# Optimization experiments

Hardware: AMD Instinct MI355X
Metric: run time of the kernel (lower is better)

## Reference

```python
import jax, jax.numpy as jnp
import numpy as np

B, T, U = 64, 800, 80          # batch, stroke timesteps, char sequence length
IN, H, V = 3, 400, 57          # input_dim, hidden_dim, onehot_dim (vocab)
K, G = 10, 20                  # n_window, n_gaussian
D1 = H + IN + V                # input dim of recurrent layers >= 1


def setup_inputs() -> dict:
    key = jax.random.key(0)
    ks = jax.random.split(key, 12)
    std = 0.075
    nrm = lambda k, shp: (std * jax.random.normal(k, shp)).astype(jnp.float32)
    char_ids = jax.random.randint(ks[1], (B, U), 0, V)
    return {
        "x_input": jax.random.normal(ks[0], (B, T, IN), jnp.float32),
        "onehot": jax.nn.one_hot(char_ids, V, dtype=jnp.float32),
        "h0": jnp.zeros((B, H), jnp.float32),
        "h1": jnp.zeros((B, H), jnp.float32),
        "h2": jnp.zeros((B, H), jnp.float32),
        # GRU layer 0 (input: strokes only)
        "W_ih0": nrm(ks[2], (3 * H, IN)), "W_hh0": nrm(ks[3], (3 * H, H)),
        "b_ih0": jnp.zeros((3 * H,), jnp.float32), "b_hh0": jnp.zeros((3 * H,), jnp.float32),
        # GRU layer 1 (shared by all layers >= 1, faithful to the torch code which
        # always calls self.rnn_layer1 in the loop)
        "W_ih1": nrm(ks[4], (3 * H, D1)), "W_hh1": nrm(ks[5], (3 * H, H)),
        "b_ih1": jnp.zeros((3 * H,), jnp.float32), "b_hh1": jnp.zeros((3 * H,), jnp.float32),
        # attention window linear: hidden -> 3*K (alpha, beta, kappa); bias ~ N(-4, 0.1)
        "W_win": nrm(ks[6], (3 * K, H)),
        "b_win": (-4.0 + 0.1 * jax.random.normal(ks[7], (3 * K,))).astype(jnp.float32),
        # MDN head: hidden -> 1 + 6*G
        "W_mdn": nrm(ks[8], (1 + 6 * G, H)),
        "b_mdn": jnp.zeros((1 + 6 * G,), jnp.float32),
    }


def gru(x, h0, W_ih, W_hh, b_ih, b_hh):
    """PyTorch-convention GRU. x: (B,T,D), h0: (B,H) -> (out (B,T,H), hT (B,H))."""
    xg = jnp.einsum('btd,gd->btg', x, W_ih) + b_ih  # (B,T,3H), precomputed input gates

    def step(h, xg_t):
        gh = h @ W_hh.T + b_hh
        xr, xz, xn = jnp.split(xg_t, 3, axis=-1)
        hr, hz, hn = jnp.split(gh, 3, axis=-1)
        r = jax.nn.sigmoid(xr + hr)
        z = jax.nn.sigmoid(xz + hz)
        n = jnp.tanh(xn + r * hn)
        h_new = (1.0 - z) * n + z * h
        return h_new, h_new

    hT, outs = jax.lax.scan(step, h0, jnp.swapaxes(xg, 0, 1))
    return jnp.swapaxes(outs, 0, 1), hT


def reference(x_input, onehot, h0, h1, h2,
              W_ih0, W_hh0, b_ih0, b_hh0,
              W_ih1, W_hh1, b_ih1, b_hh1,
              W_win, b_win, W_mdn, b_mdn):
    out0, _ = gru(x_input, h0, W_ih0, W_hh0, b_ih0, b_hh0)  # (B,T,H)

    # Graves attention window (training=True path: running_kappa = cumsum(kappa))
    abk = jnp.exp(out0 @ W_win.T + b_win)                    # (B,T,3K)
    alpha, beta, kappa = jnp.split(abk, 3, axis=-1)          # each (B,T,K)
    running_kappa = jnp.cumsum(kappa, axis=1)                # (B,T,K)
    u = jnp.arange(onehot.shape[1], dtype=x_input.dtype)     # (U,)
    diff = running_kappa[..., None] - u                      # (B,T,K,U)
    phi = jnp.sum(alpha[..., None] * jnp.exp(-beta[..., None] * diff * diff), axis=2)  # (B,T,U)
    window = jnp.einsum('btu,buv->btv', phi, onehot)         # (B,T,V)

    # layers >= 1 all use layer-1 weights (faithful to original torch code)
    out = jnp.concatenate([out0, window, x_input], axis=-1)
    out, _ = gru(out, h1, W_ih1, W_hh1, b_ih1, b_hh1)
    out = jnp.concatenate([out, window, x_input], axis=-1)
    out, _ = gru(out, h2, W_ih1, W_hh1, b_ih1, b_hh1)

    mdn = out.reshape(-1, H) @ W_mdn.T + b_mdn               # (B*T, 1+6G)
    pi_logit = mdn[:, 0 * G:1 * G]
    mu1 = mdn[:, 1 * G:2 * G]
    mu2 = mdn[:, 2 * G:3 * G]
    log_sigma1 = mdn[:, 3 * G:4 * G]
    log_sigma2 = mdn[:, 4 * G:5 * G]
    rho = jnp.tanh(mdn[:, 5 * G:6 * G])
    e_logit = mdn[:, 6 * G:]
    return jnp.concatenate([pi_logit, mu1, mu2, log_sigma1, log_sigma2, rho, e_logit], axis=-1)
```

## Files before the change

### kernel.cpp

```cpp
#include <hip/hip_runtime.h>
#include <math.h>

#define Bx 64
#define Tx 800
#define Ux 80
#define INx 3
#define Hx 400
#define Vx 57
#define Kx 10


typedef float v2f __attribute__((ext_vector_type(2)));
typedef float v4f __attribute__((ext_vector_type(4)));

__device__ __forceinline__ float sigf(float x) { return 1.f / (1.f + expf(-x)); }

__device__ __forceinline__ void pk_lo(v2f& acc, v2f w, v2f h) {
    asm("v_pk_fma_f32 %0, %1, %2, %0 op_sel:[0,0,0] op_sel_hi:[0,1,1]"
        : "+v"(acc) : "v"(w), "v"(h));
}
__device__ __forceinline__ void pk_hi(v2f& acc, v2f w, v2f h) {
    asm("v_pk_fma_f32 %0, %1, %2, %0 op_sel:[1,0,0] op_sel_hi:[1,1,1]"
        : "+v"(acc) : "v"(w), "v"(h));
}

__global__ void k_zero(int* __restrict__ cnt) {
    int i = blockIdx.x * blockDim.x + threadIdx.x;
    if (i < 3 * 16 * 32) cnt[i] = 0;
}

__global__ void k_transpose_x(const float* __restrict__ x, float* __restrict__ xT) {
    int idx = blockIdx.x * blockDim.x + threadIdx.x;
    if (idx >= Tx * INx * Bx) return;
    int b = idx & 63;
    int d = (idx >> 6) % INx;
    int t = idx / (64 * INx);
    xT[idx] = x[((size_t)b * Tx + t) * INx + d];
}

__global__ void k_transpose_oh(const float* __restrict__ oh, float* __restrict__ ohT) {
    int idx = blockIdx.x * blockDim.x + threadIdx.x;
    if (idx >= Ux * Vx * Bx) return;
    int b = idx & 63;
    int uv = idx >> 6;
    int v = uv % Vx;
    int u = uv / Vx;
    ohT[idx] = oh[((size_t)b * Ux + u) * Vx + v];
}

__global__ void k_packW(const float* __restrict__ Whh, const float* __restrict__ Wih,
                        float* __restrict__ Wp, int NP, int xcols) {
    int idx = blockIdx.x * blockDim.x + threadIdx.x;
    int total = 16 * 3 * NP * 400;
    if (idx >= total) return;
    int q = idx % 400;
    int m = (idx / 400) % (3 * NP);
    int us = idx / (400 * 3 * NP);
    int g = m / NP, p = m % NP;
    int s = q / 25, u = q % 25;
    int row = g * 400 + us * 25 + u;
    float v0, v1;
    if (p < 13) {
        int kl0 = 2 * p, kl1 = 2 * p + 1;
        v0 = (kl0 < 25) ? Whh[(size_t)row * 400 + s * 25 + kl0] : 0.f;
        v1 = (kl1 < 25) ? Whh[(size_t)row * 400 + s * 25 + kl1] : 0.f;
    } else {
        int jx0 = 2 * (p - 13), jx1 = jx0 + 1;
        int kx0 = s * 29 + jx0, kx1 = s * 29 + jx1;
        v0 = (jx0 < 29 && kx0 < xcols) ? Wih[(size_t)row * xcols + kx0] : 0.f;
        v1 = (jx1 < 29 && kx1 < xcols) ? Wih[(size_t)row * xcols + kx1] : 0.f;
    }
    Wp[(size_t)idx * 2]     = v0;
    Wp[(size_t)idx * 2 + 1] = v1;
}

template <int XP>
__global__ __launch_bounds__(448, 1) void k_rec(
    const float* __restrict__ Wp, const float* __restrict__ prev,
    const float* __restrict__ winb, const float* __restrict__ xT,
    const float* __restrict__ hinit, const float* __restrict__ Wih_small,
    const float* __restrict__ bih, const float* __restrict__ bhh,
    float* __restrict__ outL, int* __restrict__ cnt) {
    constexpr int NP = 13 + XP;
    constexpr int XW = (XP > 0) ? 466 : 4;
    __shared__ __align__(16) float xcat_h[404 * 4];
    __shared__ __align__(16) float xcat_x[2][XW * 4];
    __shared__ __align__(16) float hprev[2][104 * 4];
    __shared__ v2f red2[8 * 400];
    __shared__ float biasLDS[150];
    __shared__ float wih0LDS[225];

    const int tid = threadIdx.x;
    const int us = blockIdx.x & 15;
    const int cg = blockIdx.x >> 4;
    const int cb = cg * 4;
    const int U0 = us * 25;
    const int q = tid;
    const int s = q / 25;
    int* cnt_cg = cnt + cg * 32;

    v2f wr[NP], wz[NP], wn[NP];
    if (q < 400) {
        const v2f* Wp2 = (const v2f*)Wp;
        const size_t base = (size_t)(us * 3 * NP) * 400 + q;
        #pragma unroll
        for (int m = 0; m < NP; ++m) {
            wr[m] = Wp2[base + (size_t)m * 400];
            wz[m] = Wp2[base + (size_t)(NP + m) * 400];
            wn[m] = Wp2[base + (size_t)(2 * NP + m) * 400];
        }
    } else {
        #pragma unroll
        for (int m = 0; m < NP; ++m) {
            wr[m] = (v2f){0.f, 0.f}; wz[m] = (v2f){0.f, 0.f}; wn[m] = (v2f){0.f, 0.f};
        }
    }
    #pragma unroll
    for (int m = 0; m < NP; ++m) {
        asm volatile("" : "+v"(wr[m]));
        asm volatile("" : "+v"(wz[m]));
        asm volatile("" : "+v"(wn[m]));
    }
    if (tid < 75)        biasLDS[tid] = bih[(tid / 25) * 400 + U0 + (tid % 25)];
    else if (tid < 150)  biasLDS[tid] = bhh[((tid - 75) / 25) * 400 + U0 + ((tid - 75) % 25)];
    if (XP == 0 && tid < 225) {
        int u = tid / 9, r9 = tid % 9, g = r9 / 3, d = r9 % 3;
        wih0LDS[tid] = Wih_small[(size_t)(g * 400 + U0 + u) * 3 + d];
    }
    for (int k = tid; k < 404; k += 448)
        *(v4f*)&xcat_h[k * 4] = (v4f){0.f, 0.f, 0.f, 0.f};
    for (int k = tid; k < 2 * XW; k += 448)
        *(v4f*)&xcat_x[0][k * 4] = (v4f){0.f, 0.f, 0.f, 0.f};

    if (XP > 0) {
        for (int kx = tid; kx < 460; kx += 448) {
            v4f xv;
            if (kx < 400)      xv = *(const v4f*)(prev + (size_t)kx * 64 + cb);
            else if (kx < 457) xv = *(const v4f*)(winb + (size_t)(kx - 400) * 64 + cb);
            else               xv = *(const v4f*)(xT + (size_t)(kx - 457) * 64 + cb);
            *(v4f*)&xcat_x[0][kx * 4] = xv;
        }
    } else {
        if (tid < 3)
            *(v4f*)&xcat_x[0][tid * 4] = *(const v4f*)(xT + (size_t)tid * 64 + cb);
    }

    for (int t = 0; t < Tx; ++t) {
        const int pl = t & 1;
        if (t > 0) {
            if (tid < 64) {
                int* fp = cnt_cg + (tid & 15);
                int fv = __hip_atomic_load(fp, __ATOMIC_RELAXED, __HIP_MEMORY_SCOPE_AGENT);
                while (!__all(fv >= t)) {
                    __builtin_amdgcn_s_sleep(1);
                    fv = __hip_atomic_load(fp, __ATOMIC_RELAXED, __HIP_MEMORY_SCOPE_AGENT);
                }
            }
            __syncthreads();
        }
        if (tid < 400) {
            v4f hv;
            if (t == 0) {
                hv.x = hinit[(size_t)(cb + 0) * 400 + tid];
                hv.y = hinit[(size_t)(cb + 1) * 400 + tid];
                hv.z = hinit[(size_t)(cb + 2) * 400 + tid];
                hv.w = hinit[(size_t)(cb + 3) * 400 + tid];
            } else {
                const float* hp0 = outL + (size_t)(t - 1) * 25600 + (size_t)tid * 64 + cb;
                asm volatile("global_load_dwordx4 %0, %1, off sc0 sc1"
                             : "=v"(hv) : "v"(hp0) : "memory");
                asm volatile("s_waitcnt vmcnt(0)" ::: "memory");
            }
            *(v4f*)&xcat_h[tid * 4] = hv;
            int d = tid - U0;
            if ((unsigned)d < 25u) *(v4f*)&hprev[t & 1][d * 4] = hv;
        }
        __syncthreads();

        if (q < 400) {
            v2f aR0 = {0, 0}, aR1 = {0, 0}, aZ0 = {0, 0}, aZ1 = {0, 0};
            v2f aHN0 = {0, 0}, aHN1 = {0, 0}, aXN0 = {0, 0}, aXN1 = {0, 0};
            const float* hb = &xcat_h[s * 100];
            #pragma unroll
            for (int p = 0; p < 13; ++p) {
                v2f a01 = *(const v2f*)(hb + 8 * p);
                v2f a23 = *(const v2f*)(hb + 8 * p + 2);
                v2f b01 = *(const v2f*)(hb + 8 * p + 4);
                v2f b23 = *(const v2f*)(hb + 8 * p + 6);
                v2f r_ = wr[p], z_ = wz[p], n_ = wn[p];
                pk_lo(aR0, r_, a01);  pk_lo(aR1, r_, a23);
                pk_hi(aR0, r_, b01);  pk_hi(aR1, r_, b23);
                pk_lo(aZ0, z_, a01);  pk_lo(aZ1, z_, a23);
                pk_hi(aZ0, z_, b01);  pk_hi(aZ1, z_, b23);
                pk_lo(aHN0, n_, a01); pk_lo(aHN1, n_, a23);
                pk_hi(aHN0, n_, b01); pk_hi(aHN1, n_, b23);
            }
            if (XP > 0) {
                const float* xb = &xcat_x[pl][s * 29 * 4];
                #pragma unroll
                for (int p = 0; p < XP; ++p) {
                    v2f a01 = *(const v2f*)(xb + 8 * p);
                    v2f a23 = *(const v2f*)(xb + 8 * p + 2);
                    v2f b01 = *(const v2f*)(xb + 8 * p + 4);
                    v2f b23 = *(const v2f*)(xb + 8 * p + 6);
                    v2f r_ = wr[13 + p], z_ = wz[13 + p], n_ = wn[13 + p];
                    pk_lo(aR0, r_, a01);  pk_lo(aR1, r_, a23);
                    pk_hi(aR0, r_, b01);  pk_hi(aR1, r_, b23);
                    pk_lo(aZ0, z_, a01);  pk_lo(aZ1, z_, a23);
                    pk_hi(aZ0, z_, b01);  pk_hi(aZ1, z_, b23);
                    pk_lo(aXN0, n_, a01); pk_lo(aXN1, n_, a23);
                    pk_hi(aXN0, n_, b01); pk_hi(aXN1, n_, b23);
                }
            }
            red2[0 * 400 + q] = aR0;  red2[1 * 400 + q] = aR1;
            red2[2 * 400 + q] = aZ0;  red2[3 * 400 + q] = aZ1;
            red2[4 * 400 + q] = aHN0; red2[5 * 400 + q] = aHN1;
            red2[6 * 400 + q] = aXN0; red2[7 * 400 + q] = aXN1;
        }
        __syncthreads();

        if (tid < 64) {
            #pragma unroll
            for (int rep = 0; rep < 2; ++rep) {
                int o = tid + rep * 64;
                if (o < 100) {
                    int u = o >> 2, c = o & 3;
                    int half = c >> 1, e = c & 1;
                    const float* redf = (const float*)red2;
                    float R = 0, Z = 0, HN = 0, XN = 0;
                    #pragma unroll 4
                    for (int s2 = 0; s2 < 16; ++s2) {
                        int idx = s2 * 25 + u;
                        R  += redf[((0 + half) * 400 + idx) * 2 + e];
                        Z  += redf[((2 + half) * 400 + idx) * 2 + e];
                        HN += redf[((4 + half) * 400 + idx) * 2 + e];
                        XN += redf[((6 + half) * 400 + idx) * 2 + e];
                    }
                    R += biasLDS[u] + biasLDS[75 + u];
                    Z += biasLDS[25 + u] + biasLDS[100 + u];
                    XN += biasLDS[50 + u];
                    HN += biasLDS[125 + u];
                    if (XP == 0) {
                        #pragma unroll
                        for (int d = 0; d < 3; ++d) {
                            float xv = xcat_x[pl][d * 4 + c];
                            R  += wih0LDS[u * 9 + 0 + d] * xv;
                            Z  += wih0LDS[u * 9 + 3 + d] * xv;
                            XN += wih0LDS[u * 9 + 6 + d] * xv;
                        }
                    }
                    float r = sigf(R);
                    float z = sigf(Z);
                    float n = tanhf(XN + r * HN);
                    float hp = hprev[t & 1][u * 4 + c];
                    float hnew = (1.f - z) * n + z * hp;
                    __hip_atomic_store(outL + (size_t)t * 25600 + (size_t)(U0 + u) * 64 + cb + c,
                                       hnew, __ATOMIC_RELAXED, __HIP_MEMORY_SCOPE_AGENT);
                }
            }
            asm volatile("s_waitcnt vmcnt(0)" ::: "memory");
            if (tid == 0)
                __hip_atomic_store(cnt_cg + us, t + 1,
                                   __ATOMIC_RELAXED, __HIP_MEMORY_SCOPE_AGENT);
        } else if (t + 1 < Tx) {
            const int p2 = (t + 1) & 1;
            if (XP > 0) {
                for (int kx = tid - 64; kx < 460; kx += 384) {
                    v4f xv;
                    if (kx < 400)      xv = *(const v4f*)(prev + (size_t)(t + 1) * 25600 + kx * 64 + cb);
                    else if (kx < 457) xv = *(const v4f*)(winb + (size_t)(t + 1) * 3648 + (kx - 400) * 64 + cb);
                    else               xv = *(const v4f*)(xT + (size_t)(t + 1) * 192 + (kx - 457) * 64 + cb);
                    *(v4f*)&xcat_x[p2][kx * 4] = xv;
                }
            } else {
                if (tid < 67) {
                    int d = tid - 64;
                    *(v4f*)&xcat_x[p2][d * 4] = *(const v4f*)(xT + (size_t)(t + 1) * 192 + d * 64 + cb);
                }
            }
        }
    }
}

__global__ __launch_bounds__(256) void k_abk(const float* __restrict__ out0,
    const float* __restrict__ Wwin, const float* __restrict__ bwin,
    float* __restrict__ abk) {
    int t = blockIdx.x;
    int b = threadIdx.x & 63;
    int js = threadIdx.x >> 6;
    int j0 = js * 8;
    int nj = min(8, 30 - j0);
    float acc[8];
    for (int i = 0; i < nj; i++) acc[i] = bwin[j0 + i];
    const float* o = out0 + (size_t)t * 25600;
    for (int k = 0; k < Hx; k++) {
        float hv = o[k * 64 + b];
        for (int i = 0; i < nj; i++) acc[i] += Wwin[(j0 + i) * Hx + k] * hv;
    }
    for (int i = 0; i < nj; i++)
        abk[(size_t)t * 1920 + (j0 + i) * 64 + b] = expf(acc[i]);
}

__global__ void k_cumsum(float* __restrict__ abk) {
    int tid = blockIdx.x * blockDim.x + threadIdx.x;
    if (tid >= Kx * Bx) return;
    int b = tid & 63;
    int k = tid >> 6;
    float run = 0.f;
    size_t base = (size_t)(20 + k) * 64 + b;
    for (int t = 0; t < Tx; t++) {
        size_t i = (size_t)t * 1920 + base;
        run += abk[i];
        abk[i] = run;
    }
}

__global__ __launch_bounds__(256) void k_window(const float* __restrict__ abk,
    const float* __restrict__ ohT, float* __restrict__ win) {
    int t = blockIdx.x;
    int b = threadIdx.x & 63;
    int sub = threadIdx.x >> 6;
    __shared__ float phi[Ux][64];

    float al[Kx], be[Kx], kc[Kx];
    const float* ab = abk + (size_t)t * 1920;
    #pragma unroll
    for (int k = 0; k < Kx; k++) {
        al[k] = ab[k * 64 + b];
        be[k] = ab[(10 + k) * 64 + b];
        kc[k] = ab[(20 + k) * 64 + b];
    }
    for (int u = sub * 20; u < sub * 20 + 20; u++) {
        float ssum = 0.f;
        float uf = (float)u;
        #pragma unroll
        for (int k = 0; k < Kx; k++) {
            float d = kc[k] - uf;
            ssum += al[k] * __expf(-be[k] * d * d);
        }
        phi[u][b] = ssum;
    }
    __syncthreads();

    int v0 = sub * 15;
    int nv = min(15, Vx - v0);
    float acc[15];
    for (int i = 0; i < nv; i++) acc[i] = 0.f;
    for (int u = 0; u < Ux; u++) {
        float pv = phi[u][b];
        const float* oh = ohT + (size_t)(u * Vx) * 64;
        for (int i = 0; i < nv; i++) acc[i] += pv * oh[(v0 + i) * 64 + b];
    }
    for (int i = 0; i < nv; i++)
        win[(size_t)t * 3648 + (v0 + i) * 64 + b] = acc[i];
}

__global__ __launch_bounds__(256) void k_mdn(const float* __restrict__ out2,
    const float* __restrict__ Wm, const float* __restrict__ bm,
    float* __restrict__ out) {
    int t = blockIdx.x;
    int b = threadIdx.x & 63;
    int js = threadIdx.x >> 6;
    int j0 = js * 31;
    int nj = min(31, 121 - j0);
    float acc[31];
    for (int i = 0; i < nj; i++) acc[i] = bm[j0 + i];
    const float* o = out2 + (size_t)t * 25600;
    for (int k = 0; k < Hx; k += 4) {
        float i0 = o[k * 64 + b];
        float i1 = o[(k + 1) * 64 + b];
        float i2 = o[(k + 2) * 64 + b];
        float i3 = o[(k + 3) * 64 + b];
        for (int i = 0; i < nj; i++) {
            const float* wp = Wm + (size_t)(j0 + i) * Hx + k;
            float4 qv = *(const float4*)wp;
            acc[i] += qv.x * i0 + qv.y * i1 + qv.z * i2 + qv.w * i3;
        }
    }
    size_t rb = ((size_t)b * Tx + t) * 121;
    for (int i = 0; i < nj; i++) {
        int j = j0 + i;
        float v = acc[i];
        if (j >= 100 && j < 120) v = tanhf(v);
        out[rb + j] = v;
    }
}

extern "C" void kernel_launch(void* const* d_in, const int* in_sizes, int n_in,
                              void* d_out, int out_size, void* d_ws, size_t ws_size,
                              hipStream_t stream) {
    const float* x    = (const float*)d_in[0];
    const float* oneh = (const float*)d_in[1];
    const float* h0i  = (const float*)d_in[2];
    const float* h1i  = (const float*)d_in[3];
    const float* h2i  = (const float*)d_in[4];
    const float* Wih0 = (const float*)d_in[5];
    const float* Whh0 = (const float*)d_in[6];
    const float* bih0 = (const float*)d_in[7];
    const float* bhh0 = (const float*)d_in[8];
    const float* Wih1 = (const float*)d_in[9];
    const float* Whh1 = (const float*)d_in[10];
    const float* bih1 = (const float*)d_in[11];
    const float* bhh1 = (const float*)d_in[12];
    const float* Wwin = (const float*)d_in[13];
    const float* bwin = (const float*)d_in[14];
    const float* Wmdn = (const float*)d_in[15];
    const float* bmdn = (const float*)d_in[16];

    float* ws    = (float*)d_ws;
    float* out0  = ws;
    float* out12 = ws + 20480000;
    float* winb  = ws + 40960000;
    float* abk   = ws + 43878400;
    float* xT    = ws + 45414400;
    float* ohT   = ws + 45568000;
    float* Wp0   = ws + 45859840;
    float* Wp12  = ws + 46359040;
    int*   cnt   = (int*)(ws + 47434240);

    hipLaunchKernelGGL(k_zero, dim3(6), dim3(256), 0, stream, cnt);
    hipLaunchKernelGGL(k_transpose_x, dim3((Tx * INx * Bx + 255) / 256), dim3(256), 0, stream, x, xT);
    hipLaunchKernelGGL(k_transpose_oh, dim3((Ux * Vx * Bx + 255) / 256), dim3(256), 0, stream, oneh, ohT);
    hipLaunchKernelGGL(k_packW, dim3((16 * 3 * 13 * 400 + 255) / 256), dim3(256), 0, stream,
                       Whh0, Wih0, Wp0, 13, 3);
    hipLaunchKernelGGL(k_packW, dim3((16 * 3 * 28 * 400 + 255) / 256), dim3(256), 0, stream,
                       Whh1, Wih1, Wp12, 28, 460);

    hipLaunchKernelGGL((k_rec<0>), dim3(256), dim3(448), 0, stream,
                       Wp0, (const float*)nullptr, (const float*)nullptr, xT,
                       h0i, Wih0, bih0, bhh0, out0, cnt + 0 * 512);

    hipLaunchKernelGGL(k_abk, dim3(Tx), dim3(256), 0, stream, out0, Wwin, bwin, abk);
    hipLaunchKernelGGL(k_cumsum, dim3(10), dim3(64), 0, stream, abk);
    hipLaunchKernelGGL(k_window, dim3(Tx), dim3(256), 0, stream, abk, ohT, winb);

    hipLaunchKernelGGL((k_rec<15>), dim3(256), dim3(448), 0, stream,
                       Wp12, out0, winb, xT, h1i, (const float*)nullptr,
                       bih1, bhh1, out12, cnt + 1 * 512);
    hipLaunchKernelGGL((k_rec<15>), dim3(256), dim3(448), 0, stream,
                       Wp12, out12, winb, xT, h2i, (const float*)nullptr,
                       bih1, bhh1, out0, cnt + 2 * 512);

    hipLaunchKernelGGL(k_mdn, dim3(Tx), dim3(256), 0, stream, out0, Wmdn, bmdn, (float*)d_out);
}
```

Before: 13.39 ms.

## Fuse GRU layers 1 and 2 into one wavefront-pipelined persistent kernel

Layers 1 and 2 of the GRU recurrence now run concurrently in a single 512-block launch. Each layer-2 block spins on layer-1 progress counters so that it stays about two timesteps behind layer 1, rather than waiting for layer 1 to finish all 800 steps. Layer-2 reads of layer-1 output use cache-bypassing loads, and the old generic k_rec path loses its XP>0 branches. This needs all 512 blocks to be co-resident to avoid deadlock, and it puts more pressure on the memory system through the cross-layer polling.

```diff
diff --git a/kernel.cpp b/kernel.cpp
--- a/kernel.cpp
+++ b/kernel.cpp
@@ -22,6 +22,23 @@
 __device__ __forceinline__ void pk_hi(v2f& acc, v2f w, v2f h) {
     asm("v_pk_fma_f32 %0, %1, %2, %0 op_sel:[1,0,0] op_sel_hi:[1,1,1]"
         : "+v"(acc) : "v"(w), "v"(h));
+}
+
+__device__ __forceinline__ v4f load1_sc(const float* p) {
+    v4f r;
+    asm volatile("global_load_dwordx4 %0, %1, off sc0 sc1\n\t"
+                 "s_waitcnt vmcnt(0)"
+                 : "=v"(r) : "v"(p) : "memory");
+    return r;
+}
+__device__ __forceinline__ void load2_sc(v4f& a, v4f& b,
+                                         const float* pa, const float* pb) {
+    asm volatile("global_load_dwordx4 %0, %2, off sc0 sc1\n\t"
+                 "global_load_dwordx4 %1, %3, off sc0 sc1\n\t"
+                 "s_waitcnt vmcnt(0)"
+                 : "=&v"(a), "=&v"(b)
+                 : "v"(pa), "v"(pb)
+                 : "memory");
 }
 
 __global__ void k_zero(int* __restrict__ cnt) {
@@ -115,12 +132,6 @@
             wr[m] = (v2f){0.f, 0.f}; wz[m] = (v2f){0.f, 0.f}; wn[m] = (v2f){0.f, 0.f};
         }
     }
-    #pragma unroll
-    for (int m = 0; m < NP; ++m) {
-        asm volatile("" : "+v"(wr[m]));
-        asm volatile("" : "+v"(wz[m]));
-        asm volatile("" : "+v"(wn[m]));
-    }
     if (tid < 75)        biasLDS[tid] = bih[(tid / 25) * 400 + U0 + (tid % 25)];
     else if (tid < 150)  biasLDS[tid] = bhh[((tid - 75) / 25) * 400 + U0 + ((tid - 75) % 25)];
     if (XP == 0 && tid < 225) {
@@ -132,15 +143,7 @@
     for (int k = tid; k < 2 * XW; k += 448)
         *(v4f*)&xcat_x[0][k * 4] = (v4f){0.f, 0.f, 0.f, 0.f};
 
-    if (XP > 0) {
-        for (int kx = tid; kx < 460; kx += 448) {
-            v4f xv;
-            if (kx < 400)      xv = *(const v4f*)(prev + (size_t)kx * 64 + cb);
-            else if (kx < 457) xv = *(const v4f*)(winb + (size_t)(kx - 400) * 64 + cb);
-            else               xv = *(const v4f*)(xT + (size_t)(kx - 457) * 64 + cb);
-            *(v4f*)&xcat_x[0][kx * 4] = xv;
-        }
-    } else {
+    if (XP == 0) {
         if (tid < 3)
             *(v4f*)&xcat_x[0][tid * 4] = *(const v4f*)(xT + (size_t)tid * 64 + cb);
     }
@@ -166,10 +169,7 @@
                 hv.z = hinit[(size_t)(cb + 2) * 400 + tid];
                 hv.w = hinit[(size_t)(cb + 3) * 400 + tid];
             } else {
-                const float* hp0 = outL + (size_t)(t - 1) * 25600 + (size_t)tid * 64 + cb;
-                asm volatile("global_load_dwordx4 %0, %1, off sc0 sc1"
-                             : "=v"(hv) : "v"(hp0) : "memory");
-                asm volatile("s_waitcnt vmcnt(0)" ::: "memory");
+                hv = load1_sc(outL + (size_t)(t - 1) * 25600 + (size_t)tid * 64 + cb);
             }
             *(v4f*)&xcat_h[tid * 4] = hv;
             int d = tid - U0;
@@ -194,23 +194,6 @@
                 pk_hi(aZ0, z_, b01);  pk_hi(aZ1, z_, b23);
                 pk_lo(aHN0, n_, a01); pk_lo(aHN1, n_, a23);
                 pk_hi(aHN0, n_, b01); pk_hi(aHN1, n_, b23);
-            }
-            if (XP > 0) {
-                const float* xb = &xcat_x[pl][s * 29 * 4];
-                #pragma unroll
-                for (int p = 0; p < XP; ++p) {
-                    v2f a01 = *(const v2f*)(xb + 8 * p);
-                    v2f a23 = *(const v2f*)(xb + 8 * p + 2);
-                    v2f b01 = *(const v2f*)(xb + 8 * p + 4);
-                    v2f b23 = *(const v2f*)(xb + 8 * p + 6);
-                    v2f r_ = wr[13 + p], z_ = wz[13 + p], n_ = wn[13 + p];
-                    pk_lo(aR0, r_, a01);  pk_lo(aR1, r_, a23);
-                    pk_hi(aR0, r_, b01);  pk_hi(aR1, r_, b23);
-                    pk_lo(aZ0, z_, a01);  pk_lo(aZ1, z_, a23);
-                    pk_hi(aZ0, z_, b01);  pk_hi(aZ1, z_, b23);
-                    pk_lo(aXN0, n_, a01); pk_lo(aXN1, n_, a23);
-                    pk_hi(aXN0, n_, b01); pk_hi(aXN1, n_, b23);
-                }
             }
             red2[0 * 400 + q] = aR0;  red2[1 * 400 + q] = aR1;
             red2[2 * 400 + q] = aZ0;  red2[3 * 400 + q] = aZ1;
@@ -263,19 +246,225 @@
                 __hip_atomic_store(cnt_cg + us, t + 1,
                                    __ATOMIC_RELAXED, __HIP_MEMORY_SCOPE_AGENT);
         } else if (t + 1 < Tx) {
-            const int p2 = (t + 1) & 1;
-            if (XP > 0) {
-                for (int kx = tid - 64; kx < 460; kx += 384) {
-                    v4f xv;
-                    if (kx < 400)      xv = *(const v4f*)(prev + (size_t)(t + 1) * 25600 + kx * 64 + cb);
-                    else if (kx < 457) xv = *(const v4f*)(winb + (size_t)(t + 1) * 3648 + (kx - 400) * 64 + cb);
-                    else               xv = *(const v4f*)(xT + (size_t)(t + 1) * 192 + (kx - 457) * 64 + cb);
-                    *(v4f*)&xcat_x[p2][kx * 4] = xv;
-                }
-            } else {
+            if (XP == 0) {
                 if (tid < 67) {
                     int d = tid - 64;
-                    *(v4f*)&xcat_x[p2][d * 4] = *(const v4f*)(xT + (size_t)(t + 1) * 192 + d * 64 + cb);
+                    *(v4f*)&xcat_x[(t + 1) & 1][d * 4] =
+                        *(const v4f*)(xT + (size_t)(t + 1) * 192 + d * 64 + cb);
+                }
+            }
+        }
+    }
+}
+
+__device__ __forceinline__ const float* xaddr(int kx, int tt, int cb,
+    const float* prev, const float* winb, const float* xT) {
+    if (kx < 400)      return prev + (size_t)tt * 25600 + (size_t)kx * 64 + cb;
+    else if (kx < 457) return winb + (size_t)tt * 3648 + (size_t)(kx - 400) * 64 + cb;
+    else               return xT   + (size_t)tt * 192  + (size_t)(kx - 457) * 64 + cb;
+}
+
+__global__ __attribute__((amdgpu_flat_work_group_size(448, 448), amdgpu_waves_per_eu(4)))
+void k_rec12(
+    const float* __restrict__ Wp, float* __restrict__ out0,
+    float* __restrict__ out12, const float* __restrict__ winb,
+    const float* __restrict__ xT, const float* __restrict__ h1i,
+    const float* __restrict__ h2i, const float* __restrict__ bih,
+    const float* __restrict__ bhh, int* __restrict__ cnt) {
+    constexpr int NP = 28;
+    constexpr int XW = 466;
+    __shared__ __align__(16) float xcat_h[404 * 4];
+    __shared__ __align__(16) float xcat_x[2][XW * 4];
+    __shared__ __align__(16) float hprev[2][104 * 4];
+    __shared__ v2f red2[8 * 400];
+    __shared__ float biasLDS[150];
+
+    const int tid = threadIdx.x;
+    const int lay = blockIdx.x >> 8;
+    const int blk = blockIdx.x & 255;
+    const int us = blk & 15;
+    const int cg = blk >> 4;
+    const int cb = cg * 4;
+    const int U0 = us * 25;
+    const int q = tid;
+    const int s = q / 25;
+
+    const float* prev  = lay ? out12 : out0;
+    float* outL        = lay ? out0  : out12;
+    const float* hinit = lay ? h2i   : h1i;
+    int* cntOwn = cnt + (lay ? 1024 : 512) + cg * 32;
+    int* cntDep = cnt + 512 + cg * 32;
+
+    v2f wr[NP], wz[NP], wn[NP];
+    if (q < 400) {
+        const v2f* Wp2 = (const v2f*)Wp;
+        const size_t base = (size_t)(us * 3 * NP) * 400 + q;
+        #pragma unroll
+        for (int m = 0; m < NP; ++m) {
+            wr[m] = Wp2[base + (size_t)m * 400];
+            wz[m] = Wp2[base + (size_t)(NP + m) * 400];
+            wn[m] = Wp2[base + (size_t)(2 * NP + m) * 400];
+        }
+    } else {
+        #pragma unroll
+        for (int m = 0; m < NP; ++m) {
+            wr[m] = (v2f){0.f, 0.f}; wz[m] = (v2f){0.f, 0.f}; wn[m] = (v2f){0.f, 0.f};
+        }
+    }
+    if (tid < 75)        biasLDS[tid] = bih[(tid / 25) * 400 + U0 + (tid % 25)];
+    else if (tid < 150)  biasLDS[tid] = bhh[((tid - 75) / 25) * 400 + U0 + ((tid - 75) % 25)];
+    for (int k = tid; k < 404; k += 448)
+        *(v4f*)&xcat_h[k * 4] = (v4f){0.f, 0.f, 0.f, 0.f};
+    for (int k = tid; k < 2 * XW; k += 448)
+        *(v4f*)&xcat_x[0][k * 4] = (v4f){0.f, 0.f, 0.f, 0.f};
+
+    for (int t = 0; t < Tx; ++t) {
+        const int pl = t & 1;
+        if (t > 0 || lay) {
+            if (tid < 64) {
+                int i16 = tid & 15;
+                const bool mine = ((tid >> 4) & 1) == 0;
+                int* fp = mine ? (cntOwn + i16) : (cntDep + i16);
+                int tdep = t + 2; if (tdep > Tx) tdep = Tx;
+                const int tgt = mine ? t : tdep;
+                const bool active = mine ? (t > 0) : (lay != 0);
+                for (;;) {
+                    int fv = active ? __hip_atomic_load(fp, __ATOMIC_RELAXED, __HIP_MEMORY_SCOPE_AGENT)
+                                    : 0x7fffffff;
+                    if (__all(fv >= tgt)) break;
+                    __builtin_amdgcn_s_sleep(1);
+                }
+            }
+            __syncthreads();
+        }
+        if (t == 0) {
+            int kx0 = tid, kx1 = tid + 448;
+            const bool hb2 = kx1 < 460;
+            if (lay) {
+                const float* pa = xaddr(kx0, 0, cb, prev, winb, xT);
+                const float* pb = xaddr(hb2 ? kx1 : kx0, 0, cb, prev, winb, xT);
+                v4f a, b2;
+                load2_sc(a, b2, pa, pb);
+                *(v4f*)&xcat_x[0][kx0 * 4] = a;
+                if (hb2) *(v4f*)&xcat_x[0][kx1 * 4] = b2;
+            } else {
+                v4f a = *(const v4f*)xaddr(kx0, 0, cb, prev, winb, xT);
+                *(v4f*)&xcat_x[0][kx0 * 4] = a;
+                if (hb2) {
+                    v4f b2 = *(const v4f*)xaddr(kx1, 0, cb, prev, winb, xT);
+                    *(v4f*)&xcat_x[0][kx1 * 4] = b2;
+                }
+            }
+        }
+        if (tid < 400) {
+            v4f hv;
+            if (t == 0) {
+                hv.x = hinit[(size_t)(cb + 0) * 400 + tid];
+                hv.y = hinit[(size_t)(cb + 1) * 400 + tid];
+                hv.z = hinit[(size_t)(cb + 2) * 400 + tid];
+                hv.w = hinit[(size_t)(cb + 3) * 400 + tid];
+            } else {
+                hv = load1_sc(outL + (size_t)(t - 1) * 25600 + (size_t)tid * 64 + cb);
+            }
+            *(v4f*)&xcat_h[tid * 4] = hv;
+            int d = tid - U0;
+            if ((unsigned)d < 25u) *(v4f*)&hprev[t & 1][d * 4] = hv;
+        }
+        __syncthreads();
+
+        if (q < 400) {
+            v2f aR0 = {0, 0}, aR1 = {0, 0}, aZ0 = {0, 0}, aZ1 = {0, 0};
+            v2f aHN0 = {0, 0}, aHN1 = {0, 0}, aXN0 = {0, 0}, aXN1 = {0, 0};
+            const float* hb = &xcat_h[s * 100];
+            #pragma unroll
+            for (int p = 0; p < 13; ++p) {
+                v2f a01 = *(const v2f*)(hb + 8 * p);
+                v2f a23 = *(const v2f*)(hb + 8 * p + 2);
+                v2f b01 = *(const v2f*)(hb + 8 * p + 4);
+                v2f b23 = *(const v2f*)(hb + 8 * p + 6);
+                v2f r_ = wr[p], z_ = wz[p], n_ = wn[p];
+                pk_lo(aR0, r_, a01);  pk_lo(aR1, r_, a23);
+                pk_hi(aR0, r_, b01);  pk_hi(aR1, r_, b23);
+                pk_lo(aZ0, z_, a01);  pk_lo(aZ1, z_, a23);
+                pk_hi(aZ0, z_, b01);  pk_hi(aZ1, z_, b23);
+                pk_lo(aHN0, n_, a01); pk_lo(aHN1, n_, a23);
+                pk_hi(aHN0, n_, b01); pk_hi(aHN1, n_, b23);
+            }
+            {
+                const float* xb = &xcat_x[pl][s * 29 * 4];
+                #pragma unroll
+                for (int p = 0; p < 15; ++p) {
+                    v2f a01 = *(const v2f*)(xb + 8 * p);
+                    v2f a23 = *(const v2f*)(xb + 8 * p + 2);
+                    v2f b01 = *(const v2f*)(xb + 8 * p + 4);
+                    v2f b23 = *(const v2f*)(xb + 8 * p + 6);
+                    v2f r_ = wr[13 + p], z_ = wz[13 + p], n_ = wn[13 + p];
+                    pk_lo(aR0, r_, a01);  pk_lo(aR1, r_, a23);
+                    pk_hi(aR0, r_, b01);  pk_hi(aR1, r_, b23);
+                    pk_lo(aZ0, z_, a01);  pk_lo(aZ1, z_, a23);
+                    pk_hi(aZ0, z_, b01);  pk_hi(aZ1, z_, b23);
+                    pk_lo(aXN0, n_, a01); pk_lo(aXN1, n_, a23);
+                    pk_hi(aXN0, n_, b01); pk_hi(aXN1, n_, b23);
+                }
+            }
+            red2[0 * 400 + q] = aR0;  red2[1 * 400 + q] = aR1;
+            red2[2 * 400 + q] = aZ0;  red2[3 * 400 + q] = aZ1;
+            red2[4 * 400 + q] = aHN0; red2[5 * 400 + q] = aHN1;
+            red2[6 * 400 + q] = aXN0; red2[7 * 400 + q] = aXN1;
+        }
+        __syncthreads();
+
+        if (tid < 64) {
+            #pragma unroll
+            for (int rep = 0; rep < 2; ++rep) {
+                int o = tid + rep * 64;
+                if (o < 100) {
+                    int u = o >> 2, c = o & 3;
+                    int half = c >> 1, e = c & 1;
+                    const float* redf = (const float*)red2;
+                    float R = 0, Z = 0, HN = 0, XN = 0;
+                    #pragma unroll 4
+                    for (int s2 = 0; s2 < 16; ++s2) {
+                        int idx = s2 * 25 + u;
+                        R  += redf[((0 + half) * 400 + idx) * 2 + e];
+                        Z  += redf[((2 + half) * 400 + idx) * 2 + e];
+                        HN += redf[((4 + half) * 400 + idx) * 2 + e];
+                        XN += redf[((6 + half) * 400 + idx) * 2 + e];
+                    }
+                    R += biasLDS[u] + biasLDS[75 + u];
+                    Z += biasLDS[25 + u] + biasLDS[100 + u];
+                    XN += biasLDS[50 + u];
+                    HN += biasLDS[125 + u];
+                    float r = sigf(R);
+                    float z = sigf(Z);
+                    float n = tanhf(XN + r * HN);
+                    float hp = hprev[t & 1][u * 4 + c];
+                    float hnew = (1.f - z) * n + z * hp;
+                    __hip_atomic_store(outL + (size_t)t * 25600 + (size_t)(U0 + u) * 64 + cb + c,
+                                       hnew, __ATOMIC_RELAXED, __HIP_MEMORY_SCOPE_AGENT);
+                }
+            }
+            asm volatile("s_waitcnt vmcnt(0)" ::: "memory");
+            if (tid == 0)
+                __hip_atomic_store(cntOwn + us, t + 1,
+                                   __ATOMIC_RELAXED, __HIP_MEMORY_SCOPE_AGENT);
+        } else if (t + 1 < Tx) {
+            const int p2 = (t + 1) & 1;
+            int kx0 = tid - 64, kx1 = kx0 + 384;
+            const bool hb2 = kx1 < 460;
+            if (lay) {
+                const float* pa = xaddr(kx0, t + 1, cb, prev, winb, xT);
+                const float* pb = xaddr(hb2 ? kx1 : kx0, t + 1, cb, prev, winb, xT);
+                v4f a, b2;
+                load2_sc(a, b2, pa, pb);
+                *(v4f*)&xcat_x[p2][kx0 * 4] = a;
+                if (hb2) *(v4f*)&xcat_x[p2][kx1 * 4] = b2;
+            } else {
+                v4f a = *(const v4f*)xaddr(kx0, t + 1, cb, prev, winb, xT);
+                *(v4f*)&xcat_x[p2][kx0 * 4] = a;
+                if (hb2) {
+                    v4f b2 = *(const v4f*)xaddr(kx1, t + 1, cb, prev, winb, xT);
+                    *(v4f*)&xcat_x[p2][kx1 * 4] = b2;
                 }
             }
         }
@@ -434,12 +623,9 @@
     hipLaunchKernelGGL(k_cumsum, dim3(10), dim3(64), 0, stream, abk);
     hipLaunchKernelGGL(k_window, dim3(Tx), dim3(256), 0, stream, abk, ohT, winb);
 
-    hipLaunchKernelGGL((k_rec<15>), dim3(256), dim3(448), 0, stream,
-                       Wp12, out0, winb, xT, h1i, (const float*)nullptr,
-                       bih1, bhh1, out12, cnt + 1 * 512);
-    hipLaunchKernelGGL((k_rec<15>), dim3(256), dim3(448), 0, stream,
-                       Wp12, out12, winb, xT, h2i, (const float*)nullptr,
-                       bih1, bhh1, out0, cnt + 2 * 512);
+    hipLaunchKernelGGL(k_rec12, dim3(512), dim3(448), 0, stream,
+                       Wp12, out0, out12, winb, xT, h1i, h2i,
+                       bih1, bhh1, cnt);
 
     hipLaunchKernelGGL(k_mdn, dim3(Tx), dim3(256), 0, stream, out0, Wmdn, bmdn, (float*)d_out);
 }
```

After: 19.82 ms. 1.48x slower.
